# Kernel optimization log

Measured on AMD Instinct MI355X. Metric: run time of the kernel, lower is better.

The kernel has to match this reference:

```python
import jax, jax.numpy as jnp
from jax import lax
import numpy as np

B, C, H, W = 4, 256, 64, 64
CQK = C // 8  # 32


def conv3x3(x, w, b):
    # x: [B,C_in,H,W], w: [C_out,C_in,3,3], b: [C_out]
    y = lax.conv_general_dilated(x, w, window_strides=(1, 1), padding='SAME',
                                 dimension_numbers=('NCHW', 'OIHW', 'NCHW'))
    return y + b[None, :, None, None]


def setup_inputs() -> dict:
    key = jax.random.key(0)
    ks = jax.random.split(key, 8)
    scale = 0.02
    return {
        'x': jax.random.normal(ks[0], (B, C, H, W), dtype=jnp.float32),
        'wq': jax.random.normal(ks[1], (CQK, C, 3, 3), dtype=jnp.float32) * scale,
        'bq': jax.random.normal(ks[2], (CQK,), dtype=jnp.float32) * scale,
        'wk': jax.random.normal(ks[3], (CQK, C, 3, 3), dtype=jnp.float32) * scale,
        'bk': jax.random.normal(ks[4], (CQK,), dtype=jnp.float32) * scale,
        'wv': jax.random.normal(ks[5], (C, C, 3, 3), dtype=jnp.float32) * scale,
        'bv': jax.random.normal(ks[6], (C,), dtype=jnp.float32) * scale,
        'gamma': jax.random.normal(ks[7], (1,), dtype=jnp.float32) * scale,
    }


def reference(x, wq, bq, wk, bk, wv, bv, gamma):
    b, c, h, w = x.shape
    n = h * w
    # Q: [B, N, C//8]  (permute(0,2,1) of the flattened conv output)
    q = conv3x3(x, wq, bq).reshape(b, -1, n).transpose(0, 2, 1)
    # K: [B, C//8, N]
    k = conv3x3(x, wk, bk).reshape(b, -1, n)
    # s: [B, N_q, N_k]
    s = jnp.einsum('bqd,bdk->bqk', q, k)
    # NOTE: original uses Softmax(dim=-2), i.e. over the QUERY axis
    attn_T = jax.nn.softmax(s, axis=-2)
    # V: [B, C, N]
    v = conv3x3(x, wv, bv).reshape(b, c, n)
    # o = bmm(V, attn_T): [B, C, N]
    o = jnp.einsum('bcq,bqk->bck', v, attn_T).reshape(b, c, h, w)
    return x + gamma * o
```

## Files before the change

kernel.cpp:

```cpp
#include <hip/hip_runtime.h>
#include <cstddef>

#define N_PIX 4096
#define HW 64
#define LOG2E 1.4426950408889634f
#define SHIFT2 28.8539008177793f

typedef __attribute__((ext_vector_type(8))) short bf16x8;
typedef __attribute__((ext_vector_type(4))) float f32x4;

static __device__ __forceinline__ unsigned short f2bf(float f) {
    union { float f; unsigned u; } v; v.f = f;
    unsigned r = v.u + 0x7fffu + ((v.u >> 16) & 1u);
    return (unsigned short)(r >> 16);
}
static __device__ __forceinline__ float bf2f(unsigned short s) {
    union { unsigned u; float f; } v; v.u = (unsigned)s << 16;
    return v.f;
}
static __device__ __forceinline__ unsigned pack_bf16_trunc(float lo, float hi) {
    union { float f; unsigned u; } a, b; a.f = hi; b.f = lo;
    return __builtin_amdgcn_perm(a.u, b.u, 0x07060302u);
}

__global__ __launch_bounds__(256) void x_transpose(
    const float* __restrict__ x, unsigned short* __restrict__ xbf)
{
    __shared__ unsigned short Ts[64][72];
    const int tid = threadIdx.x;
    const int px0 = blockIdx.x * 64, ci0 = blockIdx.y * 64, b = blockIdx.z;
    const float* xb = x + ((size_t)b * 256 + ci0) * N_PIX;

#pragma unroll
    for (int r = 0; r < 4; ++r) {
        int c = r * 16 + (tid >> 4);
        int p4 = (tid & 15) * 4;
        float4 v = *(const float4*)&xb[(size_t)c * N_PIX + px0 + p4];
        Ts[c][p4 + 0] = f2bf(v.x);
        Ts[c][p4 + 1] = f2bf(v.y);
        Ts[c][p4 + 2] = f2bf(v.z);
        Ts[c][p4 + 3] = f2bf(v.w);
    }
    __syncthreads();
#pragma unroll
    for (int r = 0; r < 2; ++r) {
        int id = tid * 2 + r;
        int p = id >> 3, c8 = (id & 7) * 8;
        ushort4 lo, hi;
        lo.x = Ts[c8 + 0][p]; lo.y = Ts[c8 + 1][p];
        lo.z = Ts[c8 + 2][p]; lo.w = Ts[c8 + 3][p];
        hi.x = Ts[c8 + 4][p]; hi.y = Ts[c8 + 5][p];
        hi.z = Ts[c8 + 6][p]; hi.w = Ts[c8 + 7][p];
        size_t off = ((size_t)b * N_PIX + px0 + p) * 256 + ci0 + c8;
        *(ushort4*)&xbf[off]     = lo;
        *(ushort4*)&xbf[off + 4] = hi;
    }
}

__global__ __launch_bounds__(256) void w_transform(
    const float* __restrict__ wq, const float* __restrict__ wk,
    const float* __restrict__ wv, unsigned short* __restrict__ wAll)
{
    int gid = blockIdx.x * 256 + threadIdx.x;
    if (gid >= 72 * 320 * 4) return;
    int part = gid & 3;
    int m = (gid >> 2) % 320;
    int kb = gid / 1280;
    int t = kb >> 3;
    int ci0 = (kb & 7) * 32 + part * 8;
    const float* src; int co; float sc = 1.f;
    if (m < 256)      { src = wv; co = m; }
    else if (m < 288) { src = wq; co = m - 256; sc = LOG2E; }
    else              { src = wk; co = m - 288; }
    ushort4 lo, hi;
    lo.x = f2bf(sc * src[((size_t)co * 256 + ci0 + 0) * 9 + t]);
    lo.y = f2bf(sc * src[((size_t)co * 256 + ci0 + 1) * 9 + t]);
    lo.z = f2bf(sc * src[((size_t)co * 256 + ci0 + 2) * 9 + t]);
    lo.w = f2bf(sc * src[((size_t)co * 256 + ci0 + 3) * 9 + t]);
    hi.x = f2bf(sc * src[((size_t)co * 256 + ci0 + 4) * 9 + t]);
    hi.y = f2bf(sc * src[((size_t)co * 256 + ci0 + 5) * 9 + t]);
    hi.z = f2bf(sc * src[((size_t)co * 256 + ci0 + 6) * 9 + t]);
    hi.w = f2bf(sc * src[((size_t)co * 256 + ci0 + 7) * 9 + t]);
    size_t off = ((size_t)kb * 320 + m) * 32 + part * 8;
    *(ushort4*)&wAll[off]     = lo;
    *(ushort4*)&wAll[off + 4] = hi;
}

__global__ __launch_bounds__(256) void conv_gemm_v2(
    const unsigned short* __restrict__ xbf, const unsigned short* __restrict__ wAll,
    const float* __restrict__ bq, const float* __restrict__ bk,
    const float* __restrict__ bv,
    unsigned short* __restrict__ vbf, unsigned short* __restrict__ qt,
    unsigned short* __restrict__ kt)
{
    const int tid = threadIdx.x;
    const int w = tid >> 6, lane = tid & 63, quad = lane >> 4, l15 = lane & 15;
    const int px0 = blockIdx.x * 128;
    const int mt  = blockIdx.y;
    const int b   = blockIdx.z;
    const bool qk = (mt == 2);
    const int row0 = qk ? 256 : mt * 128;
    const int NCB  = qk ? 2 : 4;
    const int wc0  = (w & 1) * (qk ? 32 : 64);
    const int wp0  = (w >> 1) * 64;

    __shared__ unsigned short Bl[2][128 * 40];

    const unsigned short* xb = xbf + (size_t)b * N_PIX * 256;

    const int brow = tid >> 1;
    const int bp0  = (tid & 1) * 2;
    const int bswz = (brow >> 2) & 3;
    const int py = (px0 + brow) >> 6, pxc = brow & 63;

    f32x4 acc[4][4];
#pragma unroll
    for (int cb = 0; cb < 4; ++cb)
#pragma unroll
        for (int jb = 0; jb < 4; ++jb) acc[cb][jb] = (f32x4){0.f, 0.f, 0.f, 0.f};

    const unsigned short* aBase = wAll + ((size_t)(row0 + wc0 + l15) * 32 + quad * 8);

    auto load_a = [&](int kb, bf16x8* af) {
        const unsigned short* p = aBase + (size_t)kb * (320 * 32);
#pragma unroll
        for (int cb = 0; cb < 4; ++cb)
            if (cb < NCB) af[cb] = *(const bf16x8*)&p[cb * 512];
    };

    bf16x8 bS[2];
    auto load_b = [&](int kb) {
        int t = kb >> 3, ci0 = (kb & 7) << 5;
        int dy = t / 3 - 1, dx = t - (t / 3) * 3 - 1;
        int gy = py + dy, gx = pxc + dx;
        if ((unsigned)gy < 64u && (unsigned)gx < 64u) {
            const unsigned short* s = xb + ((size_t)(gy * 64 + gx) * 256 + ci0 + bp0 * 8);
            bS[0] = *(const bf16x8*)&s[0];
            bS[1] = *(const bf16x8*)&s[8];
        } else {
            bS[0] = (bf16x8){0,0,0,0,0,0,0,0};
            bS[1] = (bf16x8){0,0,0,0,0,0,0,0};
        }
    };
    auto store_b = [&](int buf) {
        int p0 = (bp0 + bswz) & 3;
        int p1 = (bp0 + 1 + bswz) & 3;
        *(bf16x8*)&Bl[buf][brow * 40 + p0 * 8] = bS[0];
        *(bf16x8*)&Bl[buf][brow * 40 + p1 * 8] = bS[1];
    };

    bf16x8 afC[4], afN[4];
    load_a(0, afC);
    load_b(0);
    store_b(0);

    for (int kb = 0; kb < 72; ++kb) {
        __syncthreads();
        const bool hasN = (kb + 1 < 72);
        if (hasN) { load_b(kb + 1); load_a(kb + 1, afN); }

        bf16x8 bf[4];
#pragma unroll
        for (int jb = 0; jb < 4; ++jb) {
            int row = wp0 + jb * 16 + l15;
            int pp = (quad + (row >> 2)) & 3;
            bf[jb] = *(const bf16x8*)&Bl[kb & 1][row * 40 + pp * 8];
        }
#pragma unroll
        for (int cb = 0; cb < 4; ++cb)
            if (cb < NCB)
#pragma unroll
                for (int jb = 0; jb < 4; ++jb)
                    acc[cb][jb] = __builtin_amdgcn_mfma_f32_16x16x32_bf16(
                        afC[cb], bf[jb], acc[cb][jb], 0, 0, 0);

        if (hasN) {
            store_b((kb + 1) & 1);
#pragma unroll
            for (int cb = 0; cb < 4; ++cb) afC[cb] = afN[cb];
        }
    }

    if (!qk) {
#pragma unroll
        for (int cb = 0; cb < 4; ++cb) {
            int c = mt * 128 + wc0 + cb * 16 + quad * 4;
#pragma unroll
            for (int r = 0; r < 4; ++r) {
                float bias = bv[c + r];
#pragma unroll
                for (int jb = 0; jb < 4; ++jb) {
                    int px = px0 + wp0 + jb * 16 + l15;
                    vbf[((size_t)b * 256 + c + r) * N_PIX + px] = f2bf(acc[cb][jb][r] + bias);
                }
            }
        }
    } else {
#pragma unroll
        for (int cb = 0; cb < 2; ++cb) {
            int cl = wc0 + cb * 16 + quad * 4;
#pragma unroll
            for (int r = 0; r < 4; ++r) {
                int c = cl + r;
                float bias = (c < 32) ? bq[c] * LOG2E : bk[c - 32];
#pragma unroll
                for (int jb = 0; jb < 4; ++jb) {
                    int px = px0 + wp0 + jb * 16 + l15;
                    unsigned short val = f2bf(acc[cb][jb][r] + bias);
                    if (c < 32)
                        qt[((size_t)b * N_PIX + px) * 32 + c] = val;
                    else
                        kt[((size_t)b * N_PIX + px) * 32 + (c - 32)] = val;
                }
            }
        }
    }
}

__global__ __launch_bounds__(256, 2) void fused_attn_mfma(
    const unsigned short* __restrict__ qt, const unsigned short* __restrict__ kt,
    const unsigned short* __restrict__ vbf,
    unsigned short* __restrict__ Abuf, float* __restrict__ lbuf, int iRange)
{
    const int tid  = threadIdx.x;
    const int w    = tid >> 6;
    const int lane = tid & 63;
    const int quad = lane >> 4;
    const int l15  = lane & 15;
    const int j0   = blockIdx.x * 128;
    const int b    = blockIdx.y;
    const int sp   = blockIdx.z;
    const int iBeg = sp * iRange;
    const int NI   = iRange / 64;

    const unsigned short* qtb = qt + (size_t)b * N_PIX * 32;
    const unsigned short* ktb = kt + (size_t)b * N_PIX * 32;
    const unsigned short* vb  = vbf + (size_t)b * 256 * N_PIX;

    __shared__ unsigned Pfrag[2][4096];
    __shared__ float lred[4][128];

    bf16x8 kf[8];
#pragma unroll
    for (int jb = 0; jb < 8; ++jb)
        kf[jb] = *(const bf16x8*)&ktb[((size_t)(j0 + jb * 16 + l15)) * 32 + quad * 8];

    f32x4 acc[4][8];
#pragma unroll
    for (int cb = 0; cb < 4; ++cb)
#pragma unroll
        for (int jb = 0; jb < 8; ++jb)
            acc[cb][jb] = (f32x4){0.f, 0.f, 0.f, 0.f};

    float lpart[8] = {0.f, 0.f, 0.f, 0.f, 0.f, 0.f, 0.f, 0.f};

    const int wFrag = w >> 1;
    const int wL    = ((w & 1) << 5) + ((quad >> 1) << 4) + l15;
    const int wEl2  = (quad & 1) << 1;

    bf16x8 va[2][4];

    auto s_phase = [&](bf16x8 qa, int buf) {
#pragma unroll
        for (int jb = 0; jb < 8; ++jb) {
            f32x4 s = __builtin_amdgcn_mfma_f32_16x16x32_bf16(
                qa, kf[jb], (f32x4){-SHIFT2, -SHIFT2, -SHIFT2, -SHIFT2}, 0, 0, 0);
            float p0 = __builtin_amdgcn_exp2f(s[0]);
            float p1 = __builtin_amdgcn_exp2f(s[1]);
            float p2 = __builtin_amdgcn_exp2f(s[2]);
            float p3 = __builtin_amdgcn_exp2f(s[3]);
            lpart[jb] += (p0 + p1) + (p2 + p3);
            unsigned u0 = pack_bf16_trunc(p0, p1);
            unsigned u1 = pack_bf16_trunc(p2, p3);
            unsigned base = (((jb << 1) + wFrag) * 64 + wL) * 4 + wEl2;
            Pfrag[buf][base]     = u0;
            Pfrag[buf][base + 1] = u1;
        }
    };

    auto load_qa = [&](int i0) {
        return *(const bf16x8*)&qtb[((size_t)(i0 + w * 16 + l15)) * 32 + quad * 8];
    };
    auto load_va = [&](int i0) {
#pragma unroll
        for (int ks = 0; ks < 2; ++ks)
#pragma unroll
            for (int cb = 0; cb < 4; ++cb)
                va[ks][cb] = *(const bf16x8*)&vb[((size_t)(w * 64 + cb * 16 + l15)) * N_PIX
                                                 + i0 + ks * 32 + quad * 8];
    };

    load_va(iBeg);
    s_phase(load_qa(iBeg), 0);

    for (int n = 0; n < NI; ++n) {
        __syncthreads();
        const bool hasN = (n + 1 < NI);
        const int inext = iBeg + (n + 1) * 64;
        bf16x8 qaN;
        if (hasN) qaN = load_qa(inext);

#pragma unroll
        for (int ks = 0; ks < 2; ++ks) {
            bf16x8 pb[8];
#pragma unroll
            for (int jb = 0; jb < 8; ++jb)
                pb[jb] = *(const bf16x8*)&Pfrag[n & 1][(((jb << 1) + ks) * 64 + lane) * 4];
#pragma unroll
            for (int cb = 0; cb < 4; ++cb)
#pragma unroll
                for (int jb = 0; jb < 8; ++jb)
                    acc[cb][jb] = __builtin_amdgcn_mfma_f32_16x16x32_bf16(
                        va[ks][cb], pb[jb], acc[cb][jb], 0, 0, 0);
        }

        if (hasN) {
            load_va(inext);
            s_phase(qaN, (n + 1) & 1);
        }
    }

#pragma unroll
    for (int jb = 0; jb < 8; ++jb) {
        float v = lpart[jb];
        v += __shfl_xor(v, 16, 64);
        v += __shfl_xor(v, 32, 64);
        lpart[jb] = v;
    }
    if (lane < 16) {
#pragma unroll
        for (int jb = 0; jb < 8; ++jb)
            lred[w][jb * 16 + l15] = lpart[jb];
    }
    __syncthreads();
    if (tid < 128) {
        float s = lred[0][tid] + lred[1][tid] + lred[2][tid] + lred[3][tid];
        lbuf[((size_t)sp * 4 + b) * N_PIX + j0 + tid] = s;
    }

    unsigned short* Ab = Abuf + ((size_t)sp * 4 + b) * 256 * N_PIX;
#pragma unroll
    for (int cb = 0; cb < 4; ++cb) {
        int c = w * 64 + cb * 16 + quad * 4;
#pragma unroll
        for (int jb = 0; jb < 8; ++jb) {
            int j = j0 + jb * 16 + l15;
#pragma unroll
            for (int r = 0; r < 4; ++r)
                Ab[(size_t)(c + r) * N_PIX + j] = f2bf(acc[cb][jb][r]);
        }
    }
}

__global__ __launch_bounds__(256) void combine_kernel(
    const unsigned short* __restrict__ A, const float* __restrict__ L,
    const float* __restrict__ x, const float* __restrict__ gamma,
    float* __restrict__ out, int split)
{
    const size_t CH = (size_t)4 * 256 * N_PIX;
    size_t flat = ((size_t)blockIdx.x * 256 + threadIdx.x) * 8;
    int j = (int)(flat & (N_PIX - 1));
    int b = (int)(flat >> 20);

    float a[8] = {0.f, 0.f, 0.f, 0.f, 0.f, 0.f, 0.f, 0.f};
    float l[8] = {0.f, 0.f, 0.f, 0.f, 0.f, 0.f, 0.f, 0.f};
    for (int s = 0; s < split; ++s) {
        ushort4 av0 = *(const ushort4*)&A[flat + (size_t)s * CH];
        ushort4 av1 = *(const ushort4*)&A[flat + (size_t)s * CH + 4];
        a[0] += bf2f(av0.x); a[1] += bf2f(av0.y); a[2] += bf2f(av0.z); a[3] += bf2f(av0.w);
        a[4] += bf2f(av1.x); a[5] += bf2f(av1.y); a[6] += bf2f(av1.z); a[7] += bf2f(av1.w);
        float4 l0 = *(const float4*)&L[((size_t)s * 4 + b) * N_PIX + j];
        float4 l1 = *(const float4*)&L[((size_t)s * 4 + b) * N_PIX + j + 4];
        l[0] += l0.x; l[1] += l0.y; l[2] += l0.z; l[3] += l0.w;
        l[4] += l1.x; l[5] += l1.y; l[6] += l1.z; l[7] += l1.w;
    }
    float g = gamma[0];
    float4 x0 = *(const float4*)&x[flat];
    float4 x1 = *(const float4*)&x[flat + 4];
    float4 o0, o1;
    o0.x = x0.x + g * a[0] / l[0];
    o0.y = x0.y + g * a[1] / l[1];
    o0.z = x0.z + g * a[2] / l[2];
    o0.w = x0.w + g * a[3] / l[3];
    o1.x = x1.x + g * a[4] / l[4];
    o1.y = x1.y + g * a[5] / l[5];
    o1.z = x1.z + g * a[6] / l[6];
    o1.w = x1.w + g * a[7] / l[7];
    *(float4*)&out[flat]     = o0;
    *(float4*)&out[flat + 4] = o1;
}

extern "C" void kernel_launch(void* const* d_in, const int* in_sizes, int n_in,
                              void* d_out, int out_size, void* d_ws, size_t ws_size,
                              hipStream_t stream)
{
    const float* x     = (const float*)d_in[0];
    const float* wq    = (const float*)d_in[1];
    const float* bq    = (const float*)d_in[2];
    const float* wk    = (const float*)d_in[3];
    const float* bk    = (const float*)d_in[4];
    const float* wv    = (const float*)d_in[5];
    const float* bv    = (const float*)d_in[6];
    const float* gamma = (const float*)d_in[7];
    float* out = (float*)d_out;

    const size_t szQTel  = (size_t)4 * N_PIX * 32;
    const size_t szVBFel = (size_t)4 * 256 * N_PIX;
    const size_t szXBFel = (size_t)4 * N_PIX * 256;
    const size_t szWel   = (size_t)72 * 320 * 32;
    const size_t fixedB  = (2 * szQTel + szVBFel + szXBFel + szWel) * 2;

    int split = 4;
    while (split > 1) {
        size_t need = fixedB
                    + (size_t)split * 4 * 256 * N_PIX * 2
                    + (size_t)split * 4 * N_PIX * 4;
        if (need <= ws_size) break;
        split >>= 1;
    }

    unsigned short* Abuf = (unsigned short*)d_ws;
    float* lbuf = (float*)(Abuf + (size_t)split * 4 * 256 * N_PIX);
    unsigned short* qt   = (unsigned short*)(lbuf + (size_t)split * 4 * N_PIX);
    unsigned short* kt   = qt + szQTel;
    unsigned short* vbf  = kt + szQTel;
    unsigned short* xbf  = vbf + szVBFel;
    unsigned short* wAll = xbf + szXBFel;

    x_transpose<<<dim3(N_PIX / 64, 4, 4), 256, 0, stream>>>(x, xbf);
    w_transform<<<dim3((72 * 320 * 4 + 255) / 256), 256, 0, stream>>>(wq, wk, wv, wAll);

    conv_gemm_v2<<<dim3(N_PIX / 128, 3, 4), 256, 0, stream>>>(
        xbf, wAll, bq, bk, bv, vbf, qt, kt);

    fused_attn_mfma<<<dim3(N_PIX / 128, 4, split), 256, 0, stream>>>(
        qt, kt, vbf, Abuf, lbuf, N_PIX / split);

    combine_kernel<<<dim3((4 * 256 * N_PIX) / (256 * 8)), 256, 0, stream>>>(
        Abuf, lbuf, x, gamma, out, split);
}
```

Measured before the change: 188.2 us.

## Retile conv GEMM so each block computes all 320 output channels for 64 pixels

```diff
diff --git a/kernel.cpp b/kernel.cpp
--- a/kernel.cpp
+++ b/kernel.cpp
@@ -86,7 +86,7 @@
     *(ushort4*)&wAll[off + 4] = hi;
 }
 
-__global__ __launch_bounds__(256) void conv_gemm_v2(
+__global__ __launch_bounds__(256) void conv_gemm_v3(
     const unsigned short* __restrict__ xbf, const unsigned short* __restrict__ wAll,
     const float* __restrict__ bq, const float* __restrict__ bk,
     const float* __restrict__ bv,
@@ -95,61 +95,47 @@
 {
     const int tid = threadIdx.x;
     const int w = tid >> 6, lane = tid & 63, quad = lane >> 4, l15 = lane & 15;
-    const int px0 = blockIdx.x * 128;
-    const int mt  = blockIdx.y;
-    const int b   = blockIdx.z;
-    const bool qk = (mt == 2);
-    const int row0 = qk ? 256 : mt * 128;
-    const int NCB  = qk ? 2 : 4;
-    const int wc0  = (w & 1) * (qk ? 32 : 64);
-    const int wp0  = (w >> 1) * 64;
-
-    __shared__ unsigned short Bl[2][128 * 40];
+    const int px0 = blockIdx.x * 64;
+    const int b   = blockIdx.y;
+
+    __shared__ unsigned short Bl[2][64 * 36];
 
     const unsigned short* xb = xbf + (size_t)b * N_PIX * 256;
 
-    const int brow = tid >> 1;
-    const int bp0  = (tid & 1) * 2;
-    const int bswz = (brow >> 2) & 3;
-    const int py = (px0 + brow) >> 6, pxc = brow & 63;
-
-    f32x4 acc[4][4];
-#pragma unroll
-    for (int cb = 0; cb < 4; ++cb)
+    const int brow  = tid >> 2;
+    const int bpart = tid & 3;
+    const int py = (px0 + brow) >> 6, pxc = (px0 + brow) & 63;
+
+    f32x4 acc[5][4];
+#pragma unroll
+    for (int cb = 0; cb < 5; ++cb)
 #pragma unroll
         for (int jb = 0; jb < 4; ++jb) acc[cb][jb] = (f32x4){0.f, 0.f, 0.f, 0.f};
 
-    const unsigned short* aBase = wAll + ((size_t)(row0 + wc0 + l15) * 32 + quad * 8);
+    const unsigned short* aBase = wAll + ((size_t)(w * 80 + l15) * 32 + quad * 8);
 
     auto load_a = [&](int kb, bf16x8* af) {
         const unsigned short* p = aBase + (size_t)kb * (320 * 32);
 #pragma unroll
-        for (int cb = 0; cb < 4; ++cb)
-            if (cb < NCB) af[cb] = *(const bf16x8*)&p[cb * 512];
-    };
-
-    bf16x8 bS[2];
+        for (int cb = 0; cb < 5; ++cb)
+            af[cb] = *(const bf16x8*)&p[cb * 512];
+    };
+
+    bf16x8 bS;
     auto load_b = [&](int kb) {
         int t = kb >> 3, ci0 = (kb & 7) << 5;
         int dy = t / 3 - 1, dx = t - (t / 3) * 3 - 1;
         int gy = py + dy, gx = pxc + dx;
-        if ((unsigned)gy < 64u && (unsigned)gx < 64u) {
-            const unsigned short* s = xb + ((size_t)(gy * 64 + gx) * 256 + ci0 + bp0 * 8);
-            bS[0] = *(const bf16x8*)&s[0];
-            bS[1] = *(const bf16x8*)&s[8];
-        } else {
-            bS[0] = (bf16x8){0,0,0,0,0,0,0,0};
-            bS[1] = (bf16x8){0,0,0,0,0,0,0,0};
-        }
+        if ((unsigned)gy < 64u && (unsigned)gx < 64u)
+            bS = *(const bf16x8*)&xb[(size_t)(gy * 64 + gx) * 256 + ci0 + bpart * 8];
+        else
+            bS = (bf16x8){0,0,0,0,0,0,0,0};
     };
     auto store_b = [&](int buf) {
-        int p0 = (bp0 + bswz) & 3;
-        int p1 = (bp0 + 1 + bswz) & 3;
-        *(bf16x8*)&Bl[buf][brow * 40 + p0 * 8] = bS[0];
-        *(bf16x8*)&Bl[buf][brow * 40 + p1 * 8] = bS[1];
-    };
-
-    bf16x8 afC[4], afN[4];
+        *(bf16x8*)&Bl[buf][brow * 36 + bpart * 8] = bS;
+    };
+
+    bf16x8 afC[5], afN[5];
     load_a(0, afC);
     load_b(0);
     store_b(0);
@@ -161,56 +147,40 @@
 
         bf16x8 bf[4];
 #pragma unroll
-        for (int jb = 0; jb < 4; ++jb) {
-            int row = wp0 + jb * 16 + l15;
-            int pp = (quad + (row >> 2)) & 3;
-            bf[jb] = *(const bf16x8*)&Bl[kb & 1][row * 40 + pp * 8];
-        }
-#pragma unroll
-        for (int cb = 0; cb < 4; ++cb)
-            if (cb < NCB)
-#pragma unroll
-                for (int jb = 0; jb < 4; ++jb)
-                    acc[cb][jb] = __builtin_amdgcn_mfma_f32_16x16x32_bf16(
-                        afC[cb], bf[jb], acc[cb][jb], 0, 0, 0);
+        for (int jb = 0; jb < 4; ++jb)
+            bf[jb] = *(const bf16x8*)&Bl[kb & 1][(jb * 16 + l15) * 36 + quad * 8];
+#pragma unroll
+        for (int cb = 0; cb < 5; ++cb)
+#pragma unroll
+            for (int jb = 0; jb < 4; ++jb)
+                acc[cb][jb] = __builtin_amdgcn_mfma_f32_16x16x32_bf16(
+                    afC[cb], bf[jb], acc[cb][jb], 0, 0, 0);
 
         if (hasN) {
             store_b((kb + 1) & 1);
 #pragma unroll
-            for (int cb = 0; cb < 4; ++cb) afC[cb] = afN[cb];
-        }
-    }
-
-    if (!qk) {
-#pragma unroll
-        for (int cb = 0; cb < 4; ++cb) {
-            int c = mt * 128 + wc0 + cb * 16 + quad * 4;
-#pragma unroll
-            for (int r = 0; r < 4; ++r) {
-                float bias = bv[c + r];
-#pragma unroll
-                for (int jb = 0; jb < 4; ++jb) {
-                    int px = px0 + wp0 + jb * 16 + l15;
-                    vbf[((size_t)b * 256 + c + r) * N_PIX + px] = f2bf(acc[cb][jb][r] + bias);
-                }
-            }
-        }
-    } else {
-#pragma unroll
-        for (int cb = 0; cb < 2; ++cb) {
-            int cl = wc0 + cb * 16 + quad * 4;
-#pragma unroll
-            for (int r = 0; r < 4; ++r) {
-                int c = cl + r;
-                float bias = (c < 32) ? bq[c] * LOG2E : bk[c - 32];
-#pragma unroll
-                for (int jb = 0; jb < 4; ++jb) {
-                    int px = px0 + wp0 + jb * 16 + l15;
-                    unsigned short val = f2bf(acc[cb][jb][r] + bias);
-                    if (c < 32)
-                        qt[((size_t)b * N_PIX + px) * 32 + c] = val;
-                    else
-                        kt[((size_t)b * N_PIX + px) * 32 + (c - 32)] = val;
+            for (int cb = 0; cb < 5; ++cb) afC[cb] = afN[cb];
+        }
+    }
+
+#pragma unroll
+    for (int cb = 0; cb < 5; ++cb) {
+        int rowq = w * 80 + cb * 16 + quad * 4;
+#pragma unroll
+        for (int r = 0; r < 4; ++r) {
+            int row = rowq + r;
+#pragma unroll
+            for (int jb = 0; jb < 4; ++jb) {
+                int px = px0 + jb * 16 + l15;
+                float v = acc[cb][jb][r];
+                if (row < 256) {
+                    vbf[((size_t)b * 256 + row) * N_PIX + px] = f2bf(v + bv[row]);
+                } else if (row < 288) {
+                    int c = row - 256;
+                    qt[((size_t)b * N_PIX + px) * 32 + c] = f2bf(v + bq[c] * LOG2E);
+                } else {
+                    int c = row - 288;
+                    kt[((size_t)b * N_PIX + px) * 32 + c] = f2bf(v + bk[c]);
                 }
             }
         }
@@ -430,7 +400,7 @@
     x_transpose<<<dim3(N_PIX / 64, 4, 4), 256, 0, stream>>>(x, xbf);
     w_transform<<<dim3((72 * 320 * 4 + 255) / 256), 256, 0, stream>>>(wq, wk, wv, wAll);
 
-    conv_gemm_v2<<<dim3(N_PIX / 128, 3, 4), 256, 0, stream>>>(
+    conv_gemm_v3<<<dim3(N_PIX / 64, 4), 256, 0, stream>>>(
         xbf, wAll, bq, bk, bv, vbf, qt, kt);
 
     fused_attn_mfma<<<dim3(N_PIX / 128, 4, split), 256, 0, stream>>>(
```

Result: slower. 210.7 us (+11.9%).
